# Kernel tuning notes

Measured on AMD Instinct MI355X. Metric: run time of the kernel, lower is better.

Reference implementation:

```python
import jax, jax.numpy as jnp
import numpy as np

D_MODEL = 768
NUM_HEADS = 12
D_K = D_MODEL // NUM_HEADS
B, S = 8, 1024


def setup_inputs() -> dict:
    key = jax.random.key(0)
    ks = jax.random.split(key, 10)
    sc = 1.0 / np.sqrt(D_MODEL)
    inp = {
        'x': jax.random.normal(ks[0], (B, S, D_MODEL), dtype=jnp.float32),
        'mask': jnp.tril(jnp.ones((1, 1, S, S), dtype=jnp.int32)),
        'W_q': jax.random.normal(ks[1], (D_MODEL, D_MODEL), jnp.float32) * sc,
        'b_q': jnp.zeros((D_MODEL,), jnp.float32),
        'W_k': jax.random.normal(ks[2], (D_MODEL, D_MODEL), jnp.float32) * sc,
        'b_k': jnp.zeros((D_MODEL,), jnp.float32),
        'W_v': jax.random.normal(ks[3], (D_MODEL, D_MODEL), jnp.float32) * sc,
        'b_v': jnp.zeros((D_MODEL,), jnp.float32),
        'W_o': jax.random.normal(ks[4], (D_MODEL, D_MODEL), jnp.float32) * sc,
        'b_o': jnp.zeros((D_MODEL,), jnp.float32),
    }
    return inp


def reference(x, mask, W_q, b_q, W_k, b_k, W_v, b_v, W_o, b_o):
    b, s, d = x.shape
    # project (torch Linear: y = x @ W.T + b; here weights stored as [in, out])
    q = (x @ W_q + b_q).reshape(b, s, NUM_HEADS, D_K).transpose(0, 2, 1, 3)
    k = (x @ W_k + b_k).reshape(b, s, NUM_HEADS, D_K).transpose(0, 2, 1, 3)
    v = (x @ W_v + b_v).reshape(b, s, NUM_HEADS, D_K).transpose(0, 2, 1, 3)
    scores = jnp.einsum('bhqd,bhkd->bhqk', q, k) / jnp.sqrt(jnp.float32(D_K))
    scores = jnp.where(mask == 0, jnp.float32(-jnp.inf), scores)
    attn = jax.nn.softmax(scores, axis=-1)  # dropout: eval mode (identity)
    out = jnp.einsum('bhqk,bhkd->bhqd', attn, v)
    out = out.transpose(0, 2, 1, 3).reshape(b, s, d)
    return out @ W_o + b_o
```

## Files before the change

kernel.cpp:

```cpp
#include <hip/hip_runtime.h>
#include <hip/hip_bf16.h>
#include <stdint.h>

typedef __attribute__((ext_vector_type(8))) short short8;
typedef __attribute__((ext_vector_type(4))) short s16x4;
typedef __attribute__((ext_vector_type(4))) float f32x4;

#define GLDS16(gp, lp) __builtin_amdgcn_global_load_lds( \
    (const __attribute__((address_space(1))) void*)(gp), \
    (__attribute__((address_space(3))) void*)(lp), 16, 0, 0)

__device__ __forceinline__ unsigned short f2bf(float f) {
  union { float f; unsigned u; } v; v.f = f;
  unsigned r = v.u + 0x7FFFu + ((v.u >> 16) & 1u);
  return (unsigned short)(r >> 16);
}

__device__ __forceinline__ short bfpack(float f) {
  union { float f; unsigned u; } v; v.f = f;
  return (short)((v.u + 0x8000u) >> 16);
}

__global__ __launch_bounds__(256) void cast_x(const float* __restrict__ x,
                                              unsigned short* __restrict__ o, int n4) {
  int i = blockIdx.x * 256 + threadIdx.x;
  if (i < n4) {
    float4 v = ((const float4*)x)[i];
    union { unsigned short u[4]; unsigned long long ll; } r;
    r.u[0] = f2bf(v.x); r.u[1] = f2bf(v.y); r.u[2] = f2bf(v.z); r.u[3] = f2bf(v.w);
    ((unsigned long long*)o)[i] = r.ll;
  }
}

__global__ __launch_bounds__(256) void cast_wt(const float* __restrict__ W,
                                               unsigned short* __restrict__ Wt) {
  __shared__ float t[16][17];
  int tx = threadIdx.x, ty = threadIdx.y;
  int c0 = blockIdx.x * 16, r0 = blockIdx.y * 16;
  t[ty][tx] = W[(size_t)(r0 + ty) * 768 + c0 + tx];
  __syncthreads();
  Wt[(size_t)(c0 + ty) * 768 + r0 + tx] = f2bf(t[tx][ty]);
}

__global__ __launch_bounds__(256) void trans_v(const unsigned short* __restrict__ Vb,
                                               unsigned short* __restrict__ Vt) {
  __shared__ unsigned short t[64][65];
  int b = blockIdx.z;
  int c0 = blockIdx.x * 64, s0 = blockIdx.y * 64;
  int tx = threadIdx.x & 63, ty = threadIdx.x >> 6;
  const unsigned short* src = Vb + (size_t)b * 1024 * 768;
  unsigned short* dst = Vt + (size_t)b * 768 * 1024;
#pragma unroll
  for (int i = 0; i < 16; ++i) {
    int s = ty + 4 * i;
    t[s][tx] = src[(size_t)(s0 + s) * 768 + c0 + tx];
  }
  __syncthreads();
  const int px = (tx & ~31) | (((tx >> 2) & 3) << 3) | (((tx >> 4) & 1) << 2) | (tx & 3);
#pragma unroll
  for (int i = 0; i < 16; ++i) {
    int c = ty + 4 * i;
    dst[(size_t)(c0 + c) * 1024 + s0 + px] = t[tx][c];
  }
}

__device__ __forceinline__ void gemm_core(const unsigned short* __restrict__ A,
                                          const unsigned short* __restrict__ Bt,
                                          int row0, int col0, f32x4 acc[4][4],
                                          unsigned short* sA, unsigned short* sB) {
  const int t = threadIdx.x, l = t & 63;
  const int w = t >> 6, wr = w >> 1, wc = w & 1;
  const int lr = l & 15, lk = l >> 4;
  for (int k0 = 0; k0 < 768; k0 += 32) {
#pragma unroll
    for (int i = 0; i < 2; ++i) {
      int f = (i * 256 + t) * 8, r = f >> 5, c = f & 31;
      GLDS16(A + (size_t)(row0 + r) * 768 + k0 + c, sA + f);
      GLDS16(Bt + (size_t)(col0 + r) * 768 + k0 + c, sB + f);
    }
    __syncthreads();
    short8 af[4], bfr[4];
#pragma unroll
    for (int i = 0; i < 4; ++i) af[i] = *(const short8*)(sA + (wr * 64 + i * 16 + lr) * 32 + lk * 8);
#pragma unroll
    for (int i = 0; i < 4; ++i) bfr[i] = *(const short8*)(sB + (wc * 64 + i * 16 + lr) * 32 + lk * 8);
#pragma unroll
    for (int i = 0; i < 4; ++i)
#pragma unroll
      for (int j = 0; j < 4; ++j)
        acc[i][j] = __builtin_amdgcn_mfma_f32_16x16x32_bf16(af[i], bfr[j], acc[i][j], 0, 0, 0);
    __syncthreads();
  }
}

__global__ __launch_bounds__(256) void gemm_qkv(const unsigned short* __restrict__ A,
                                                const unsigned short* __restrict__ Bt,
                                                const float* __restrict__ bq,
                                                const float* __restrict__ bk,
                                                const float* __restrict__ bv,
                                                unsigned short* __restrict__ Qb,
                                                unsigned short* __restrict__ Kb,
                                                unsigned short* __restrict__ Vb) {
  __shared__ unsigned short sA[128 * 32];
  __shared__ unsigned short sB[128 * 32];
  const int row0 = blockIdx.x * 128, col0 = blockIdx.y * 128;
  f32x4 acc[4][4] = {};
  gemm_core(A, Bt, row0, col0, acc, sA, sB);

  const int l = threadIdx.x & 63, w = threadIdx.x >> 6;
  const int wr = w >> 1, wc = w & 1, lr = l & 15, lk = l >> 4;
  const int which = (blockIdx.y * 128) / 768;
  unsigned short* outp = which == 0 ? Qb : (which == 1 ? Kb : Vb);
  const float* bias = which == 0 ? bq : (which == 1 ? bk : bv);
  const float scale = which == 0 ? 0.18033688011112042f : 1.0f;
  const int ncb = col0 - which * 768;
#pragma unroll
  for (int i = 0; i < 4; ++i)
#pragma unroll
    for (int j = 0; j < 4; ++j) {
      int n = ncb + wc * 64 + j * 16 + lr;
      float bn = bias[n];
#pragma unroll
      for (int r = 0; r < 4; ++r) {
        int m = row0 + wr * 64 + i * 16 + lk * 4 + r;
        outp[(size_t)m * 768 + n] = f2bf((acc[i][j][r] + bn) * scale);
      }
    }
}

__global__ __launch_bounds__(256) void gemm_out(const unsigned short* __restrict__ A,
                                                const unsigned short* __restrict__ Bt,
                                                const float* __restrict__ bias,
                                                float* __restrict__ C) {
  __shared__ unsigned short sA[128 * 32];
  __shared__ unsigned short sB[128 * 32];
  const int row0 = blockIdx.x * 128, col0 = blockIdx.y * 128;
  f32x4 acc[4][4] = {};
  gemm_core(A, Bt, row0, col0, acc, sA, sB);

  const int l = threadIdx.x & 63, w = threadIdx.x >> 6;
  const int wr = w >> 1, wc = w & 1, lr = l & 15, lk = l >> 4;
#pragma unroll
  for (int i = 0; i < 4; ++i)
#pragma unroll
    for (int j = 0; j < 4; ++j) {
      int n = col0 + wc * 64 + j * 16 + lr;
      float bn = bias[n];
#pragma unroll
      for (int r = 0; r < 4; ++r) {
        int m = row0 + wr * 64 + i * 16 + lk * 4 + r;
        C[(size_t)m * 768 + n] = acc[i][j][r] + bn;
      }
    }
}

__global__ __launch_bounds__(256, 3) void attn(const unsigned short* __restrict__ Q,
                                               const unsigned short* __restrict__ Kg,
                                               const unsigned short* __restrict__ V2,
                                               unsigned short* __restrict__ O) {
  __shared__ unsigned short Kl[2][4096];
  __shared__ unsigned short Vl[2][4096];
  const int tid = threadIdx.x;
  const int l = tid & 63, w = tid >> 6;
  const int lr = l & 15, lk = l >> 4;
  const int o = blockIdx.x;
  const int b = o & 7, rem = o >> 3, pair = rem & 7, h = rem >> 3;
  const int hd = h * 64;
  const size_t bS = (size_t)b * 1024;
  const unsigned short* Kbase = Kg + bS * 768 + hd;
  const unsigned short* Vbase = V2 + ((size_t)b * 768 + hd) * 1024;
  const int rs = tid >> 3;
  const int kcol = ((tid & 7) ^ (rs & 7)) * 8;
  const int swz = (lr & 7);
  const int qloc = w * 16 + lr;

#define STAGE(BUF, T)                                                          \
  do {                                                                         \
    const size_t kv0_ = (size_t)(T) * 64;                                      \
    GLDS16(Kbase + (kv0_ + rs) * 768 + kcol, &Kl[BUF][tid * 8]);               \
    GLDS16(Kbase + (kv0_ + rs + 32) * 768 + kcol, &Kl[BUF][(256 + tid) * 8]);  \
    GLDS16(Vbase + (size_t)rs * 1024 + kv0_ + kcol, &Vl[BUF][tid * 8]);        \
    GLDS16(Vbase + (size_t)(rs + 32) * 1024 + kv0_ + kcol,                     \
           &Vl[BUF][(256 + tid) * 8]);                                         \
  } while (0)

#pragma unroll 1
  for (int half = 0; half < 2; ++half) {
    const int qt = half ? 15 - pair : pair;
    const int qw = qt * 64 + w * 16;
    const int ntile = qt + 1;
    short8 bq0, bq1;
    {
      size_t qb = (bS + qw + lr) * 768 + hd + lk * 8;
      bq0 = *(const short8*)(Q + qb);
      bq1 = *(const short8*)(Q + qb + 32);
    }
    f32x4 oc0 = {}, oc1 = {}, oc2 = {}, oc3 = {};
    float lsum = 0.f;

    __syncthreads();
    STAGE(0, 0);

#pragma unroll 1
    for (int t = 0; t < ntile; ++t) {
      __syncthreads();
      if (t + 1 < ntile) STAGE((t + 1) & 1, t + 1);
      const unsigned short* Kb_ = Kl[t & 1];
      const unsigned short* Vb_ = Vl[t & 1];
      short8 kf00 = *(const short8*)(Kb_ + (0 * 16 + lr) * 64 + (((0 * 4 + lk) ^ swz) * 8));
      short8 kf01 = *(const short8*)(Kb_ + (0 * 16 + lr) * 64 + (((1 * 4 + lk) ^ swz) * 8));
      short8 kf10 = *(const short8*)(Kb_ + (1 * 16 + lr) * 64 + (((0 * 4 + lk) ^ swz) * 8));
      short8 kf11 = *(const short8*)(Kb_ + (1 * 16 + lr) * 64 + (((1 * 4 + lk) ^ swz) * 8));
      short8 kf20 = *(const short8*)(Kb_ + (2 * 16 + lr) * 64 + (((0 * 4 + lk) ^ swz) * 8));
      short8 kf21 = *(const short8*)(Kb_ + (2 * 16 + lr) * 64 + (((1 * 4 + lk) ^ swz) * 8));
      short8 kf30 = *(const short8*)(Kb_ + (3 * 16 + lr) * 64 + (((0 * 4 + lk) ^ swz) * 8));
      short8 kf31 = *(const short8*)(Kb_ + (3 * 16 + lr) * 64 + (((1 * 4 + lk) ^ swz) * 8));
      short8 vf00 = *(const short8*)(Vb_ + (0 * 16 + lr) * 64 + (((0 * 4 + lk) ^ swz) * 8));
      short8 vf01 = *(const short8*)(Vb_ + (0 * 16 + lr) * 64 + (((1 * 4 + lk) ^ swz) * 8));
      short8 vf10 = *(const short8*)(Vb_ + (1 * 16 + lr) * 64 + (((0 * 4 + lk) ^ swz) * 8));
      short8 vf11 = *(const short8*)(Vb_ + (1 * 16 + lr) * 64 + (((1 * 4 + lk) ^ swz) * 8));
      short8 vf20 = *(const short8*)(Vb_ + (2 * 16 + lr) * 64 + (((0 * 4 + lk) ^ swz) * 8));
      short8 vf21 = *(const short8*)(Vb_ + (2 * 16 + lr) * 64 + (((1 * 4 + lk) ^ swz) * 8));
      short8 vf30 = *(const short8*)(Vb_ + (3 * 16 + lr) * 64 + (((0 * 4 + lk) ^ swz) * 8));
      short8 vf31 = *(const short8*)(Vb_ + (3 * 16 + lr) * 64 + (((1 * 4 + lk) ^ swz) * 8));

      f32x4 s0 = {}, s1 = {}, s2 = {}, s3 = {};
      __builtin_amdgcn_s_setprio(1);
      s0 = __builtin_amdgcn_mfma_f32_16x16x32_bf16(kf00, bq0, s0, 0, 0, 0);
      s0 = __builtin_amdgcn_mfma_f32_16x16x32_bf16(kf01, bq1, s0, 0, 0, 0);
      s1 = __builtin_amdgcn_mfma_f32_16x16x32_bf16(kf10, bq0, s1, 0, 0, 0);
      s1 = __builtin_amdgcn_mfma_f32_16x16x32_bf16(kf11, bq1, s1, 0, 0, 0);
      s2 = __builtin_amdgcn_mfma_f32_16x16x32_bf16(kf20, bq0, s2, 0, 0, 0);
      s2 = __builtin_amdgcn_mfma_f32_16x16x32_bf16(kf21, bq1, s2, 0, 0, 0);
      s3 = __builtin_amdgcn_mfma_f32_16x16x32_bf16(kf30, bq0, s3, 0, 0, 0);
      s3 = __builtin_amdgcn_mfma_f32_16x16x32_bf16(kf31, bq1, s3, 0, 0, 0);
      __builtin_amdgcn_s_setprio(0);

      if (t == ntile - 1) {
        const int kb = lk * 4;
#pragma unroll
        for (int r = 0; r < 4; ++r) {
          if (kb + 0 + r > qloc) s0[r] = -1e30f;
          if (kb + 16 + r > qloc) s1[r] = -1e30f;
          if (kb + 32 + r > qloc) s2[r] = -1e30f;
          if (kb + 48 + r > qloc) s3[r] = -1e30f;
        }
      }
      float p0[4], p1[4], p2[4], p3[4];
#pragma unroll
      for (int r = 0; r < 4; ++r) {
        p0[r] = __builtin_amdgcn_exp2f(s0[r]);
        p1[r] = __builtin_amdgcn_exp2f(s1[r]);
        p2[r] = __builtin_amdgcn_exp2f(s2[r]);
        p3[r] = __builtin_amdgcn_exp2f(s3[r]);
      }
      lsum += ((p0[0] + p0[1]) + (p0[2] + p0[3])) + ((p1[0] + p1[1]) + (p1[2] + p1[3])) +
              ((p2[0] + p2[1]) + (p2[2] + p2[3])) + ((p3[0] + p3[1]) + (p3[2] + p3[3]));
      short8 pb0, pb1;
#pragma unroll
      for (int r = 0; r < 4; ++r) {
        pb0[r] = bfpack(p0[r]); pb0[r + 4] = bfpack(p1[r]);
        pb1[r] = bfpack(p2[r]); pb1[r + 4] = bfpack(p3[r]);
      }
      __builtin_amdgcn_s_setprio(1);
      oc0 = __builtin_amdgcn_mfma_f32_16x16x32_bf16(vf00, pb0, oc0, 0, 0, 0);
      oc0 = __builtin_amdgcn_mfma_f32_16x16x32_bf16(vf01, pb1, oc0, 0, 0, 0);
      oc1 = __builtin_amdgcn_mfma_f32_16x16x32_bf16(vf10, pb0, oc1, 0, 0, 0);
      oc1 = __builtin_amdgcn_mfma_f32_16x16x32_bf16(vf11, pb1, oc1, 0, 0, 0);
      oc2 = __builtin_amdgcn_mfma_f32_16x16x32_bf16(vf20, pb0, oc2, 0, 0, 0);
      oc2 = __builtin_amdgcn_mfma_f32_16x16x32_bf16(vf21, pb1, oc2, 0, 0, 0);
      oc3 = __builtin_amdgcn_mfma_f32_16x16x32_bf16(vf30, pb0, oc3, 0, 0, 0);
      oc3 = __builtin_amdgcn_mfma_f32_16x16x32_bf16(vf31, pb1, oc3, 0, 0, 0);
      __builtin_amdgcn_s_setprio(0);
    }

    lsum += __shfl_xor(lsum, 16);
    lsum += __shfl_xor(lsum, 32);
    const float inv = 1.f / lsum;
    unsigned short* op = O + (bS + qw + lr) * 768 + hd + lk * 4;
    s16x4 o0, o1, o2, o3;
#pragma unroll
    for (int r = 0; r < 4; ++r) {
      o0[r] = (short)f2bf(oc0[r] * inv);
      o1[r] = (short)f2bf(oc1[r] * inv);
      o2[r] = (short)f2bf(oc2[r] * inv);
      o3[r] = (short)f2bf(oc3[r] * inv);
    }
    *(s16x4*)(op) = o0;
    *(s16x4*)(op + 16) = o1;
    *(s16x4*)(op + 32) = o2;
    *(s16x4*)(op + 48) = o3;
  }
#undef STAGE
}

extern "C" void kernel_launch(void* const* d_in, const int* in_sizes, int n_in,
                              void* d_out, int out_size, void* d_ws, size_t ws_size,
                              hipStream_t stream) {
  const float* x  = (const float*)d_in[0];
  const float* Wq = (const float*)d_in[2]; const float* bq = (const float*)d_in[3];
  const float* Wk = (const float*)d_in[4]; const float* bk = (const float*)d_in[5];
  const float* Wv = (const float*)d_in[6]; const float* bv = (const float*)d_in[7];
  const float* Wo = (const float*)d_in[8]; const float* bo = (const float*)d_in[9];
  float* out = (float*)d_out;

  char* ws = (char*)d_ws;
  unsigned short* xb  = (unsigned short*)ws;
  unsigned short* WtQ = (unsigned short*)(ws + (size_t)12582912);
  unsigned short* WtK = WtQ + 589824;
  unsigned short* WtV = WtK + 589824;
  unsigned short* WtO = WtV + 589824;
  unsigned short* Qb  = (unsigned short*)(ws + (size_t)12582912 + (size_t)4 * 1179648);
  unsigned short* Kb  = Qb + 6291456;
  unsigned short* Vb  = Kb + 6291456;
  unsigned short* Vt  = Vb + 6291456;
  unsigned short* Ob  = xb;

  cast_x<<<6144, 256, 0, stream>>>(x, xb, 1572864);
  dim3 b16(16, 16);
  cast_wt<<<dim3(48, 48), b16, 0, stream>>>(Wq, WtQ);
  cast_wt<<<dim3(48, 48), b16, 0, stream>>>(Wk, WtK);
  cast_wt<<<dim3(48, 48), b16, 0, stream>>>(Wv, WtV);
  cast_wt<<<dim3(48, 48), b16, 0, stream>>>(Wo, WtO);
  gemm_qkv<<<dim3(64, 18), 256, 0, stream>>>(xb, WtQ, bq, bk, bv, Qb, Kb, Vb);
  trans_v<<<dim3(12, 16, 8), 256, 0, stream>>>(Vb, Vt);
  attn<<<768, 256, 0, stream>>>(Qb, Kb, Vt, Ob);
  gemm_out<<<dim3(64, 6), 256, 0, stream>>>(Ob, WtO, bo, out);
}
```

Measured before the change: 114.1 us.

## Double-buffer GEMM LDS tiles with XOR swizzle and merge weight cast launches

The shared GEMM core now uses two LDS buffers, so the next K tile's global-to-LDS load is issued while MFMAs run on the current tile. Each k-step needs one barrier instead of two. Column chunks are XOR-swizzled on the way into LDS and read back with the matching swizzle to cut bank conflicts, and MFMA issue priority is raised around the compute block. The four weight-transpose casts are merged into one launch using blockIdx.z. The trade-off is doubled LDS per block, with occupancy hinted at 3 blocks per CU.

```diff
diff --git a/kernel.cpp b/kernel.cpp
--- a/kernel.cpp
+++ b/kernel.cpp
@@ -32,9 +32,18 @@
   }
 }
 
-__global__ __launch_bounds__(256) void cast_wt(const float* __restrict__ W,
-                                               unsigned short* __restrict__ Wt) {
+__global__ __launch_bounds__(256) void cast_wt4(const float* __restrict__ W0,
+                                                const float* __restrict__ W1,
+                                                const float* __restrict__ W2,
+                                                const float* __restrict__ W3,
+                                                unsigned short* __restrict__ T0,
+                                                unsigned short* __restrict__ T1,
+                                                unsigned short* __restrict__ T2,
+                                                unsigned short* __restrict__ T3) {
   __shared__ float t[16][17];
+  const int z = blockIdx.z;
+  const float* W = z == 0 ? W0 : (z == 1 ? W1 : (z == 2 ? W2 : W3));
+  unsigned short* Wt = z == 0 ? T0 : (z == 1 ? T1 : (z == 2 ? T2 : T3));
   int tx = threadIdx.x, ty = threadIdx.y;
   int c0 = blockIdx.x * 16, r0 = blockIdx.y * 16;
   t[ty][tx] = W[(size_t)(r0 + ty) * 768 + c0 + tx];
@@ -71,41 +80,58 @@
   const int t = threadIdx.x, l = t & 63;
   const int w = t >> 6, wr = w >> 1, wc = w & 1;
   const int lr = l & 15, lk = l >> 4;
-  for (int k0 = 0; k0 < 768; k0 += 32) {
-#pragma unroll
-    for (int i = 0; i < 2; ++i) {
-      int f = (i * 256 + t) * 8, r = f >> 5, c = f & 31;
-      GLDS16(A + (size_t)(row0 + r) * 768 + k0 + c, sA + f);
-      GLDS16(Bt + (size_t)(col0 + r) * 768 + k0 + c, sB + f);
-    }
+  const int rs = t >> 2;
+  const int csw = ((t & 3) ^ (rs & 3) ^ ((t >> 4) & 3)) * 8;
+  const int rsw = (lr & 3) ^ (lr >> 2);
+  const unsigned short* Ar = A + (size_t)(row0 + rs) * 768 + csw;
+  const unsigned short* Br = Bt + (size_t)(col0 + rs) * 768 + csw;
+
+#define GSTAGE(BUF, K0)                                                     \
+  do {                                                                      \
+    GLDS16(Ar + (K0), sA + (BUF) * 4096 + t * 8);                           \
+    GLDS16(Ar + (size_t)64 * 768 + (K0), sA + (BUF) * 4096 + 2048 + t * 8); \
+    GLDS16(Br + (K0), sB + (BUF) * 4096 + t * 8);                           \
+    GLDS16(Br + (size_t)64 * 768 + (K0), sB + (BUF) * 4096 + 2048 + t * 8); \
+  } while (0)
+
+  GSTAGE(0, 0);
+#pragma unroll 1
+  for (int kt = 0; kt < 24; ++kt) {
     __syncthreads();
+    if (kt + 1 < 24) GSTAGE((kt + 1) & 1, (kt + 1) * 32);
+    const unsigned short* cA = sA + (kt & 1) * 4096;
+    const unsigned short* cB = sB + (kt & 1) * 4096;
     short8 af[4], bfr[4];
 #pragma unroll
-    for (int i = 0; i < 4; ++i) af[i] = *(const short8*)(sA + (wr * 64 + i * 16 + lr) * 32 + lk * 8);
-#pragma unroll
-    for (int i = 0; i < 4; ++i) bfr[i] = *(const short8*)(sB + (wc * 64 + i * 16 + lr) * 32 + lk * 8);
+    for (int i = 0; i < 4; ++i)
+      af[i] = *(const short8*)(cA + (wr * 64 + i * 16 + lr) * 32 + ((lk ^ rsw) * 8));
+#pragma unroll
+    for (int i = 0; i < 4; ++i)
+      bfr[i] = *(const short8*)(cB + (wc * 64 + i * 16 + lr) * 32 + ((lk ^ rsw) * 8));
+    __builtin_amdgcn_s_setprio(1);
 #pragma unroll
     for (int i = 0; i < 4; ++i)
 #pragma unroll
       for (int j = 0; j < 4; ++j)
         acc[i][j] = __builtin_amdgcn_mfma_f32_16x16x32_bf16(af[i], bfr[j], acc[i][j], 0, 0, 0);
-    __syncthreads();
-  }
-}
-
-__global__ __launch_bounds__(256) void gemm_qkv(const unsigned short* __restrict__ A,
-                                                const unsigned short* __restrict__ Bt,
-                                                const float* __restrict__ bq,
-                                                const float* __restrict__ bk,
-                                                const float* __restrict__ bv,
-                                                unsigned short* __restrict__ Qb,
-                                                unsigned short* __restrict__ Kb,
-                                                unsigned short* __restrict__ Vb) {
-  __shared__ unsigned short sA[128 * 32];
-  __shared__ unsigned short sB[128 * 32];
+    __builtin_amdgcn_s_setprio(0);
+  }
+#undef GSTAGE
+}
+
+__global__ __launch_bounds__(256, 3) void gemm_qkv(const unsigned short* __restrict__ A,
+                                                   const unsigned short* __restrict__ Bt,
+                                                   const float* __restrict__ bq,
+                                                   const float* __restrict__ bk,
+                                                   const float* __restrict__ bv,
+                                                   unsigned short* __restrict__ Qb,
+                                                   unsigned short* __restrict__ Kb,
+                                                   unsigned short* __restrict__ Vb) {
+  __shared__ unsigned short sA[2][128 * 32];
+  __shared__ unsigned short sB[2][128 * 32];
   const int row0 = blockIdx.x * 128, col0 = blockIdx.y * 128;
   f32x4 acc[4][4] = {};
-  gemm_core(A, Bt, row0, col0, acc, sA, sB);
+  gemm_core(A, Bt, row0, col0, acc, &sA[0][0], &sB[0][0]);
 
   const int l = threadIdx.x & 63, w = threadIdx.x >> 6;
   const int wr = w >> 1, wc = w & 1, lr = l & 15, lk = l >> 4;
@@ -128,15 +154,15 @@
     }
 }
 
-__global__ __launch_bounds__(256) void gemm_out(const unsigned short* __restrict__ A,
-                                                const unsigned short* __restrict__ Bt,
-                                                const float* __restrict__ bias,
-                                                float* __restrict__ C) {
-  __shared__ unsigned short sA[128 * 32];
-  __shared__ unsigned short sB[128 * 32];
+__global__ __launch_bounds__(256, 3) void gemm_out(const unsigned short* __restrict__ A,
+                                                   const unsigned short* __restrict__ Bt,
+                                                   const float* __restrict__ bias,
+                                                   float* __restrict__ C) {
+  __shared__ unsigned short sA[2][128 * 32];
+  __shared__ unsigned short sB[2][128 * 32];
   const int row0 = blockIdx.x * 128, col0 = blockIdx.y * 128;
   f32x4 acc[4][4] = {};
-  gemm_core(A, Bt, row0, col0, acc, sA, sB);
+  gemm_core(A, Bt, row0, col0, acc, &sA[0][0], &sB[0][0]);
 
   const int l = threadIdx.x & 63, w = threadIdx.x >> 6;
   const int wr = w >> 1, wc = w & 1, lr = l & 15, lk = l >> 4;
@@ -317,11 +343,7 @@
   unsigned short* Ob  = xb;
 
   cast_x<<<6144, 256, 0, stream>>>(x, xb, 1572864);
-  dim3 b16(16, 16);
-  cast_wt<<<dim3(48, 48), b16, 0, stream>>>(Wq, WtQ);
-  cast_wt<<<dim3(48, 48), b16, 0, stream>>>(Wk, WtK);
-  cast_wt<<<dim3(48, 48), b16, 0, stream>>>(Wv, WtV);
-  cast_wt<<<dim3(48, 48), b16, 0, stream>>>(Wo, WtO);
+  cast_wt4<<<dim3(48, 48, 4), dim3(16, 16), 0, stream>>>(Wq, Wk, Wv, Wo, WtQ, WtK, WtV, WtO);
   gemm_qkv<<<dim3(64, 18), 256, 0, stream>>>(xb, WtQ, bq, bk, bv, Qb, Kb, Vb);
   trans_v<<<dim3(12, 16, 8), 256, 0, stream>>>(Vb, Vt);
   attn<<<768, 256, 0, stream>>>(Qb, Kb, Vt, Ob);
```

Result: no change. 113.6 us (-0.5%).
